# Kernel tuning notes

Hardware: AMD Instinct MI355X
Metric: run time of the kernel (lower is better)

## Reference

```python
import jax, jax.numpy as jnp
import numpy as np

D_MODEL = 1024
NUM_HEADS = 16
D_K = D_MODEL // NUM_HEADS
SCALE = float(np.sqrt(D_K))


def setup_inputs() -> dict:
    key = jax.random.key(0)
    ks = jax.random.split(key, 6)
    x = jax.random.normal(ks[0], (2, 2048, D_MODEL), dtype=jnp.float32)
    s = 1.0 / np.sqrt(D_MODEL)
    w_q = jax.random.uniform(ks[1], (D_MODEL, D_MODEL), jnp.float32, -s, s)
    w_k = jax.random.uniform(ks[2], (D_MODEL, D_MODEL), jnp.float32, -s, s)
    w_v = jax.random.uniform(ks[3], (D_MODEL, D_MODEL), jnp.float32, -s, s)
    w_o = jax.random.uniform(ks[4], (D_MODEL, D_MODEL), jnp.float32, -s, s)
    b_o = jax.random.uniform(ks[5], (D_MODEL,), jnp.float32, -s, s)
    return {"x": x, "w_q": w_q, "w_k": w_k, "w_v": w_v, "w_o": w_o, "b_o": b_o}


def reference(x, w_q, w_k, w_v, w_o, b_o):
    B, S, _ = x.shape
    # project and split heads: [B, H, S, d_k]
    def heads(w):
        return (x @ w.T).reshape(B, S, NUM_HEADS, D_K).transpose(0, 2, 1, 3)
    Q, K, V = heads(w_q), heads(w_k), heads(w_v)
    scores = jnp.einsum("bhqd,bhkd->bhqk", Q, K) / SCALE  # [B,H,S,S]
    attn = jax.nn.softmax(scores, axis=-1)
    context = jnp.einsum("bhqk,bhkd->bhqd", attn, V)
    context = context.transpose(0, 2, 1, 3).reshape(B, S, D_MODEL)
    return context @ w_o.T + b_o
```

## Files before the change

kernel.cpp:

```cpp
#include <hip/hip_runtime.h>

typedef unsigned short u16t;
typedef short bf16x8 __attribute__((ext_vector_type(8)));
typedef short bf16x4 __attribute__((ext_vector_type(4)));
typedef float f32x4 __attribute__((ext_vector_type(4)));

#define NHEADS 16
#define SEQ 2048
#define DMODEL 1024
#define HEAD_ELEMS (SEQ * 64)
#define LSTR 72
#define QSTR 40
#define MATE ((size_t)2 * SEQ * DMODEL)
#define CSC 0.1803368801f
#define MB 4.0f

__device__ __forceinline__ u16t f2bf(float f) {
  union { float f; unsigned u; } v; v.f = f;
  unsigned r = v.u + 0x7FFFu + ((v.u >> 16) & 1u);
  return (u16t)(r >> 16);
}
__device__ __forceinline__ float bf2f(u16t b) {
  union { unsigned u; float f; } v; v.u = ((unsigned)b) << 16;
  return v.f;
}
__device__ __forceinline__ float sanef(float x) {
  return fminf(fmaxf(x, -16384.f), 16384.f);
}
__device__ __forceinline__ unsigned pk2(float a, float b) {
  union { float f; unsigned u; } x, y; x.f = a; y.f = b;
  return __builtin_amdgcn_perm(y.u + 0x8000u, x.u + 0x8000u, 0x07060302u);
}
__device__ __forceinline__ bf16x8 cvt8(const float* p) {
  const f32x4* q4 = (const f32x4*)p;
  f32x4 a = q4[0], b = q4[1];
  bf16x8 o;
  o[0] = (short)f2bf(a[0]); o[1] = (short)f2bf(a[1]);
  o[2] = (short)f2bf(a[2]); o[3] = (short)f2bf(a[3]);
  o[4] = (short)f2bf(b[0]); o[5] = (short)f2bf(b[1]);
  o[6] = (short)f2bf(b[2]); o[7] = (short)f2bf(b[3]);
  return o;
}

struct ushort4a { u16t x, y, z, w; } __attribute__((aligned(8)));

__device__ __forceinline__ int detect_bf16_wave(const u16t* p) {
  int lane = threadIdx.x & 63;
  int cnt = 0;
#pragma unroll
  for (int i = 0; i < 8; ++i) {
    int ex = (p[2 * (lane * 8 + i)] >> 7) & 0xFF;
    cnt += (ex >= 100 && ex <= 140) ? 1 : 0;
  }
  cnt += __shfl_xor(cnt, 1);
  cnt += __shfl_xor(cnt, 2);
  cnt += __shfl_xor(cnt, 4);
  cnt += __shfl_xor(cnt, 8);
  cnt += __shfl_xor(cnt, 16);
  cnt += __shfl_xor(cnt, 32);
  return cnt >= 300;
}

__global__ __launch_bounds__(256, 3) void qkv_kernel(
    const void* __restrict__ xv,
    const void* __restrict__ wqv, const void* __restrict__ wkv,
    const void* __restrict__ wvv,
    u16t* __restrict__ q_ws, u16t* __restrict__ k_ws, u16t* __restrict__ vt_ws) {
  __shared__ u16t As[2][128 * QSTR];
  __shared__ u16t Bs[2][128 * QSTR];
  const int bfm = detect_bf16_wave((const u16t*)xv);
  const int tid = threadIdx.x;
  const int bm0 = blockIdx.x * 128;
  const int bn0 = blockIdx.y * 128;
  const int z = blockIdx.z;
  const void* Wv = (z == 0) ? wqv : ((z == 1) ? wkv : wvv);
  const float scale = (z == 0) ? CSC : 1.0f;
  const int lane = tid & 63;
  const int w = tid >> 6;
  const int ln = lane & 15;
  const int quad = lane >> 4;
  const int wm = (w & 1) * 64;
  const int wn = (w >> 1) * 64;

  f32x4 acc[4][4] = {};

  auto do_mfma = [&](int cur) {
    bf16x8 a[4], b[4];
#pragma unroll
    for (int t = 0; t < 4; ++t)
      a[t] = *(const bf16x8*)&As[cur][(wm + t * 16 + ln) * QSTR + quad * 8];
#pragma unroll
    for (int t = 0; t < 4; ++t)
      b[t] = *(const bf16x8*)&Bs[cur][(wn + t * 16 + ln) * QSTR + quad * 8];
    if (z < 2) {
#pragma unroll
      for (int p = 0; p < 4; ++p)
#pragma unroll
        for (int q = 0; q < 4; ++q)
          acc[p][q] = __builtin_amdgcn_mfma_f32_16x16x32_bf16(b[p], a[q], acc[p][q], 0, 0, 0);
    } else {
#pragma unroll
      for (int p = 0; p < 4; ++p)
#pragma unroll
        for (int q = 0; q < 4; ++q)
          acc[p][q] = __builtin_amdgcn_mfma_f32_16x16x32_bf16(a[p], b[q], acc[p][q], 0, 0, 0);
    }
  };

  if (bfm) {
    const u16t* x = (const u16t*)xv;
    const u16t* W = (const u16t*)Wv;
    const int c0 = tid, c1 = tid + 256;
    const int r0 = c0 >> 2, o0 = (c0 & 3) * 8;
    const int r1 = c1 >> 2, o1 = (c1 & 3) * 8;
    const u16t* xa0 = x + (size_t)(bm0 + r0) * DMODEL + o0;
    const u16t* xa1 = x + (size_t)(bm0 + r1) * DMODEL + o1;
    const u16t* wb0 = W + (size_t)(bn0 + r0) * DMODEL + o0;
    const u16t* wb1 = W + (size_t)(bn0 + r1) * DMODEL + o1;
    const int d0 = r0 * QSTR + o0, d1 = r1 * QSTR + o1;

    bf16x8 ra0 = *(const bf16x8*)xa0, ra1 = *(const bf16x8*)xa1;
    bf16x8 rb0 = *(const bf16x8*)wb0, rb1 = *(const bf16x8*)wb1;
    *(bf16x8*)&As[0][d0] = ra0; *(bf16x8*)&As[0][d1] = ra1;
    *(bf16x8*)&Bs[0][d0] = rb0; *(bf16x8*)&Bs[0][d1] = rb1;
    __syncthreads();
    for (int kt = 0; kt < 32; ++kt) {
      int cur = kt & 1;
      if (kt < 31) {
        xa0 += 32; xa1 += 32; wb0 += 32; wb1 += 32;
        ra0 = *(const bf16x8*)xa0; ra1 = *(const bf16x8*)xa1;
        rb0 = *(const bf16x8*)wb0; rb1 = *(const bf16x8*)wb1;
      }
      do_mfma(cur);
      if (kt < 31) {
        int nxt = cur ^ 1;
        *(bf16x8*)&As[nxt][d0] = ra0; *(bf16x8*)&As[nxt][d1] = ra1;
        *(bf16x8*)&Bs[nxt][d0] = rb0; *(bf16x8*)&Bs[nxt][d1] = rb1;
        __syncthreads();
      }
    }
  } else {
    const float* x = (const float*)xv;
    const float* W = (const float*)Wv;
    for (int kt = 0; kt < 32; ++kt) {
      __syncthreads();
#pragma unroll
      for (int j = 0; j < 2; ++j) {
        int c = j * 256 + tid;
        int row = c >> 2, col = (c & 3) * 8;
        *(bf16x8*)&As[0][row * QSTR + col] = cvt8(x + (size_t)(bm0 + row) * DMODEL + kt * 32 + col);
        *(bf16x8*)&Bs[0][row * QSTR + col] = cvt8(W + (size_t)(bn0 + row) * DMODEL + kt * 32 + col);
      }
      __syncthreads();
      do_mfma(0);
    }
  }

  if (z < 2) {
    u16t* dst = (z == 0) ? q_ws : k_ws;
#pragma unroll
    for (int p = 0; p < 4; ++p) {
      int n_base = bn0 + wn + p * 16 + quad * 4;
      int h = n_base >> 6, dkb = n_base & 63;
#pragma unroll
      for (int q = 0; q < 4; ++q) {
        int m = bm0 + wm + q * 16 + ln;
        int bb = m >> 11, sq = m & 2047;
        ushort4a pk;
        pk.x = f2bf(sanef(acc[p][q][0]) * scale);
        pk.y = f2bf(sanef(acc[p][q][1]) * scale);
        pk.z = f2bf(sanef(acc[p][q][2]) * scale);
        pk.w = f2bf(sanef(acc[p][q][3]) * scale);
        *(ushort4a*)&dst[(size_t)(bb * NHEADS + h) * HEAD_ELEMS + sq * 64 + dkb] = pk;
      }
    }
  } else {
#pragma unroll
    for (int p = 0; p < 4; ++p) {
      int m_base = bm0 + wm + p * 16 + quad * 4;
      int bb = m_base >> 11, sq = m_base & 2047;
#pragma unroll
      for (int q = 0; q < 4; ++q) {
        int n = bn0 + wn + q * 16 + ln;
        int h = n >> 6, dk = n & 63;
        ushort4a pk;
        pk.x = f2bf(sanef(acc[p][q][0]));
        pk.y = f2bf(sanef(acc[p][q][1]));
        pk.z = f2bf(sanef(acc[p][q][2]));
        pk.w = f2bf(sanef(acc[p][q][3]));
        *(ushort4a*)&vt_ws[(size_t)(bb * NHEADS + h) * HEAD_ELEMS + (size_t)dk * SEQ + sq] = pk;
      }
    }
  }
}

__global__ __launch_bounds__(512, 4) void attn_kernel(
    const u16t* __restrict__ q_ws, const u16t* __restrict__ k_ws,
    const u16t* __restrict__ vt_ws, u16t* __restrict__ ctx_ws) {
  __shared__ u16t Ks[2][64 * LSTR];
  __shared__ u16t Vt[2][64 * LSTR];
  const int tid = threadIdx.x;
  const int w = tid >> 6;
  const int lane = tid & 63;
  const int ln = lane & 15;
  const int quad = lane >> 4;
  const int bh = blockIdx.y;
  const size_t base = (size_t)bh * HEAD_ELEMS;
  const int q0w = blockIdx.x * 128 + w * 16;

  bf16x8 aq[2];
#pragma unroll
  for (int ks = 0; ks < 2; ++ks)
    aq[ks] = *(const bf16x8*)(q_ws + base + (size_t)(q0w + ln) * 64 + ks * 32 + quad * 8);

  const int r = tid >> 3;
  const int cc = (tid & 7) * 8;
  const int d = r * LSTR + cc;
  const u16t* kp = k_ws + base + (size_t)tid * 8;
  const u16t* vp = vt_ws + base + (size_t)r * SEQ + cc;

  f32x4 accO[4] = {};
  float psum = 0.f;

  bf16x8 rk = *(const bf16x8*)kp;
  bf16x8 rv = *(const bf16x8*)vp;
  *(bf16x8*)&Ks[0][d] = rk;
  *(bf16x8*)&Vt[0][d] = rv;
  __syncthreads();

  for (int kt = 0; kt < 32; ++kt) {
    const int cur = kt & 1;
    if (kt < 31) {
      kp += 4096; vp += 64;
      rk = *(const bf16x8*)kp;
      rv = *(const bf16x8*)vp;
    }

    f32x4 st[4];
#pragma unroll
    for (int nt = 0; nt < 4; ++nt) {
      st[nt][0] = -MB; st[nt][1] = -MB; st[nt][2] = -MB; st[nt][3] = -MB;
    }
#pragma unroll
    for (int nt = 0; nt < 4; ++nt)
#pragma unroll
      for (int ks = 0; ks < 2; ++ks) {
        bf16x8 bk = *(const bf16x8*)&Ks[cur][(nt * 16 + ln) * LSTR + ks * 32 + quad * 8];
        st[nt] = __builtin_amdgcn_mfma_f32_16x16x32_bf16(bk, aq[ks], st[nt], 0, 0, 0);
      }

#pragma unroll
    for (int pp = 0; pp < 2; ++pp) {
      float pv[8];
#pragma unroll
      for (int j = 0; j < 4; ++j) {
        pv[j]     = exp2f(st[2 * pp][j]);
        pv[4 + j] = exp2f(st[2 * pp + 1][j]);
      }
      psum += ((pv[0] + pv[1]) + (pv[2] + pv[3])) + ((pv[4] + pv[5]) + (pv[6] + pv[7]));
      union { unsigned u[4]; bf16x8 v; } ap;
      ap.u[0] = pk2(pv[0], pv[1]);
      ap.u[1] = pk2(pv[2], pv[3]);
      ap.u[2] = pk2(pv[4], pv[5]);
      ap.u[3] = pk2(pv[6], pv[7]);
#pragma unroll
      for (int dt = 0; dt < 4; ++dt) {
        const u16t* vrow = &Vt[cur][(dt * 16 + ln) * LSTR + quad * 4];
        bf16x4 lo = *(const bf16x4*)(vrow + (2 * pp) * 16);
        bf16x4 hi = *(const bf16x4*)(vrow + (2 * pp + 1) * 16);
        bf16x8 bb = __builtin_shufflevector(lo, hi, 0, 1, 2, 3, 4, 5, 6, 7);
        accO[dt] = __builtin_amdgcn_mfma_f32_16x16x32_bf16(ap.v, bb, accO[dt], 0, 0, 0);
      }
    }

    if (kt < 31) {
      const int nxt = cur ^ 1;
      *(bf16x8*)&Ks[nxt][d] = rk;
      *(bf16x8*)&Vt[nxt][d] = rv;
      __syncthreads();
    }
  }

  psum += __shfl_xor(psum, 16);
  psum += __shfl_xor(psum, 32);
  float inv[4];
#pragma unroll
  for (int rr = 0; rr < 4; ++rr) {
    float lq = __shfl(psum, quad * 4 + rr);
    inv[rr] = 1.0f / fmaxf(lq, 1e-20f);
  }
#pragma unroll
  for (int dt = 0; dt < 4; ++dt)
#pragma unroll
    for (int rr = 0; rr < 4; ++rr)
      ctx_ws[base + (size_t)(q0w + quad * 4 + rr) * 64 + dt * 16 + ln] =
          f2bf(accO[dt][rr] * inv[rr]);
}

__global__ __launch_bounds__(256, 4) void outproj_kernel(
    const u16t* __restrict__ ctx, const void* __restrict__ wov,
    const void* __restrict__ bov_, void* __restrict__ outv) {
  __shared__ u16t As[2][64 * LSTR];
  __shared__ u16t Bs[2][64 * LSTR];
  const int bfm = detect_bf16_wave((const u16t*)wov);
  const int tid = threadIdx.x;
  const int bm0 = blockIdx.x * 64;
  const int bn0 = blockIdx.y * 64;
  const int lane = tid & 63;
  const int w = tid >> 6;
  const int ln = lane & 15;
  const int quad = lane >> 4;
  const int wm = (w & 1) * 32;
  const int wn = (w >> 1) * 32;

  f32x4 acc[2][2] = {};

  auto do_mfma = [&](int cur) {
    bf16x8 a[2][2], b[2][2];
#pragma unroll
    for (int t = 0; t < 2; ++t)
#pragma unroll
      for (int ks = 0; ks < 2; ++ks) {
        a[t][ks] = *(const bf16x8*)&As[cur][(wm + t * 16 + ln) * LSTR + ks * 32 + quad * 8];
        b[t][ks] = *(const bf16x8*)&Bs[cur][(wn + t * 16 + ln) * LSTR + ks * 32 + quad * 8];
      }
#pragma unroll
    for (int p = 0; p < 2; ++p)
#pragma unroll
      for (int q = 0; q < 2; ++q)
#pragma unroll
        for (int ks = 0; ks < 2; ++ks)
          acc[p][q] = __builtin_amdgcn_mfma_f32_16x16x32_bf16(b[p][ks], a[q][ks], acc[p][q], 0, 0, 0);
  };

  const int c0 = tid, c1 = tid + 256;
  const int r0 = c0 >> 3, o0 = (c0 & 7) * 8;
  const int r1 = c1 >> 3, o1 = (c1 & 7) * 8;
  const int d0 = r0 * LSTR + o0, d1 = r1 * LSTR + o1;
  const int m0 = bm0 + r0, m1 = bm0 + r1;
  const u16t* ap0 = ctx + (size_t)((m0 >> 11) * NHEADS) * HEAD_ELEMS + (m0 & 2047) * 64 + o0;
  const u16t* ap1 = ctx + (size_t)((m1 >> 11) * NHEADS) * HEAD_ELEMS + (m1 & 2047) * 64 + o1;

  if (bfm) {
    const u16t* wo = (const u16t*)wov;
    const u16t* bp0 = wo + (size_t)(bn0 + r0) * DMODEL + o0;
    const u16t* bp1 = wo + (size_t)(bn0 + r1) * DMODEL + o1;
    bf16x8 ra0 = *(const bf16x8*)ap0, ra1 = *(const bf16x8*)ap1;
    bf16x8 rb0 = *(const bf16x8*)bp0, rb1 = *(const bf16x8*)bp1;
    *(bf16x8*)&As[0][d0] = ra0; *(bf16x8*)&As[0][d1] = ra1;
    *(bf16x8*)&Bs[0][d0] = rb0; *(bf16x8*)&Bs[0][d1] = rb1;
    __syncthreads();
    for (int kt = 0; kt < 16; ++kt) {
      int cur = kt & 1;
      if (kt < 15) {
        ap0 += HEAD_ELEMS; ap1 += HEAD_ELEMS;
        bp0 += 64; bp1 += 64;
        ra0 = *(const bf16x8*)ap0; ra1 = *(const bf16x8*)ap1;
        rb0 = *(const bf16x8*)bp0; rb1 = *(const bf16x8*)bp1;
      }
      do_mfma(cur);
      if (kt < 15) {
        int nxt = cur ^ 1;
        *(bf16x8*)&As[nxt][d0] = ra0; *(bf16x8*)&As[nxt][d1] = ra1;
        *(bf16x8*)&Bs[nxt][d0] = rb0; *(bf16x8*)&Bs[nxt][d1] = rb1;
        __syncthreads();
      }
    }
  } else {
    const float* wo = (const float*)wov;
    for (int kt = 0; kt < 16; ++kt) {
      __syncthreads();
      *(bf16x8*)&As[0][d0] = *(const bf16x8*)(ap0 + (size_t)kt * HEAD_ELEMS);
      *(bf16x8*)&As[0][d1] = *(const bf16x8*)(ap1 + (size_t)kt * HEAD_ELEMS);
      *(bf16x8*)&Bs[0][d0] = cvt8(wo + (size_t)(bn0 + r0) * DMODEL + kt * 64 + o0);
      *(bf16x8*)&Bs[0][d1] = cvt8(wo + (size_t)(bn0 + r1) * DMODEL + kt * 64 + o1);
      __syncthreads();
      do_mfma(0);
    }
  }

#pragma unroll
  for (int p = 0; p < 2; ++p) {
    int n_base = bn0 + wn + p * 16 + quad * 4;
    float bv0, bv1, bv2, bv3;
    if (bfm) {
      ushort4a bb = *(const ushort4a*)&((const u16t*)bov_)[n_base];
      bv0 = bf2f(bb.x); bv1 = bf2f(bb.y); bv2 = bf2f(bb.z); bv3 = bf2f(bb.w);
    } else {
      const float* bf = (const float*)bov_;
      bv0 = bf[n_base]; bv1 = bf[n_base + 1]; bv2 = bf[n_base + 2]; bv3 = bf[n_base + 3];
    }
#pragma unroll
    for (int q = 0; q < 2; ++q) {
      int m = bm0 + wm + q * 16 + ln;
      float v0 = sanef(acc[p][q][0]) + bv0;
      float v1 = sanef(acc[p][q][1]) + bv1;
      float v2 = sanef(acc[p][q][2]) + bv2;
      float v3 = sanef(acc[p][q][3]) + bv3;
      if (bfm) {
        ushort4a pk; pk.x = f2bf(v0); pk.y = f2bf(v1); pk.z = f2bf(v2); pk.w = f2bf(v3);
        *(ushort4a*)&((u16t*)outv)[(size_t)m * DMODEL + n_base] = pk;
      } else {
        f32x4 pk; pk[0] = v0; pk[1] = v1; pk[2] = v2; pk[3] = v3;
        *(f32x4*)&((float*)outv)[(size_t)m * DMODEL + n_base] = pk;
      }
    }
  }
}

extern "C" void kernel_launch(void* const* d_in, const int* in_sizes, int n_in,
                              void* d_out, int out_size, void* d_ws, size_t ws_size,
                              hipStream_t stream) {
  (void)in_sizes; (void)n_in; (void)out_size; (void)ws_size;
  const void* x  = d_in[0];
  const void* wq = d_in[1];
  const void* wk = d_in[2];
  const void* wv = d_in[3];
  const void* wo = d_in[4];
  const void* bo = d_in[5];

  u16t* q_ws  = (u16t*)d_ws;
  u16t* k_ws  = q_ws + MATE;
  u16t* vt_ws = k_ws + MATE;
  u16t* ctx_ws = q_ws;

  dim3 gA(32, 8, 3);
  qkv_kernel<<<gA, 256, 0, stream>>>(x, wq, wk, wv, q_ws, k_ws, vt_ws);

  dim3 gB(16, 32);
  attn_kernel<<<gB, 512, 0, stream>>>(q_ws, k_ws, vt_ws, ctx_ws);

  dim3 gC(64, 16);
  outproj_kernel<<<gC, 256, 0, stream>>>(ctx_ws, wo, bo, d_out);
}
```

Before: 234.7 us.

## Retile out-projection to 128x128 with direct global-to-LDS loads, single-buffer attention

The output projection moves from 64x64 to 128x128 tiles with K-step 32. It loads A and B straight into LDS through global_load_lds, raising data reuse per block and removing register staging. The attention kernel drops its LDS double buffering in favour of a single buffer with two barriers per tile, which cuts shared memory use but exposes global load latency. The qkv launch bounds rise to 4 waves per SIMD for occupancy. These changes trade fewer blocks and less pipelining for larger tiles and lower LDS pressure.

Result: slower. 550.6 us (+134.6%).

```diff
diff --git a/kernel.cpp b/kernel.cpp
--- a/kernel.cpp
+++ b/kernel.cpp
@@ -42,6 +42,12 @@
   return o;
 }
 
+__device__ __forceinline__ void stage16(const u16t* g, u16t* l) {
+  __builtin_amdgcn_global_load_lds(
+      (const __attribute__((address_space(1))) unsigned int*)g,
+      (__attribute__((address_space(3))) unsigned int*)l, 16, 0, 0);
+}
+
 struct ushort4a { u16t x, y, z, w; } __attribute__((aligned(8)));
 
 __device__ __forceinline__ int detect_bf16_wave(const u16t* p) {
@@ -61,7 +67,7 @@
   return cnt >= 300;
 }
 
-__global__ __launch_bounds__(256, 3) void qkv_kernel(
+__global__ __launch_bounds__(256, 4) void qkv_kernel(
     const void* __restrict__ xv,
     const void* __restrict__ wqv, const void* __restrict__ wkv,
     const void* __restrict__ wvv,
@@ -197,8 +203,8 @@
 __global__ __launch_bounds__(512, 4) void attn_kernel(
     const u16t* __restrict__ q_ws, const u16t* __restrict__ k_ws,
     const u16t* __restrict__ vt_ws, u16t* __restrict__ ctx_ws) {
-  __shared__ u16t Ks[2][64 * LSTR];
-  __shared__ u16t Vt[2][64 * LSTR];
+  __shared__ u16t Ks[64 * LSTR];
+  __shared__ u16t Vt[64 * LSTR];
   const int tid = threadIdx.x;
   const int w = tid >> 6;
   const int lane = tid & 63;
@@ -215,26 +221,21 @@
 
   const int r = tid >> 3;
   const int cc = (tid & 7) * 8;
-  const int d = r * LSTR + cc;
   const u16t* kp = k_ws + base + (size_t)tid * 8;
   const u16t* vp = vt_ws + base + (size_t)r * SEQ + cc;
+  u16t* kl = &Ks[r * LSTR + cc];
+  u16t* vl = &Vt[r * LSTR + cc];
 
   f32x4 accO[4] = {};
   float psum = 0.f;
 
-  bf16x8 rk = *(const bf16x8*)kp;
-  bf16x8 rv = *(const bf16x8*)vp;
-  *(bf16x8*)&Ks[0][d] = rk;
-  *(bf16x8*)&Vt[0][d] = rv;
-  __syncthreads();
-
   for (int kt = 0; kt < 32; ++kt) {
-    const int cur = kt & 1;
-    if (kt < 31) {
-      kp += 4096; vp += 64;
-      rk = *(const bf16x8*)kp;
-      rv = *(const bf16x8*)vp;
-    }
+    bf16x8 rk = *(const bf16x8*)kp; kp += 4096;
+    bf16x8 rv = *(const bf16x8*)vp; vp += 64;
+    __syncthreads();
+    *(bf16x8*)kl = rk;
+    *(bf16x8*)vl = rv;
+    __syncthreads();
 
     f32x4 st[4];
 #pragma unroll
@@ -245,7 +246,7 @@
     for (int nt = 0; nt < 4; ++nt)
 #pragma unroll
       for (int ks = 0; ks < 2; ++ks) {
-        bf16x8 bk = *(const bf16x8*)&Ks[cur][(nt * 16 + ln) * LSTR + ks * 32 + quad * 8];
+        bf16x8 bk = *(const bf16x8*)&Ks[(nt * 16 + ln) * LSTR + ks * 32 + quad * 8];
         st[nt] = __builtin_amdgcn_mfma_f32_16x16x32_bf16(bk, aq[ks], st[nt], 0, 0, 0);
       }
 
@@ -265,20 +266,13 @@
       ap.u[3] = pk2(pv[6], pv[7]);
 #pragma unroll
       for (int dt = 0; dt < 4; ++dt) {
-        const u16t* vrow = &Vt[cur][(dt * 16 + ln) * LSTR + quad * 4];
+        const u16t* vrow = &Vt[(dt * 16 + ln) * LSTR + quad * 4];
         bf16x4 lo = *(const bf16x4*)(vrow + (2 * pp) * 16);
         bf16x4 hi = *(const bf16x4*)(vrow + (2 * pp + 1) * 16);
         bf16x8 bb = __builtin_shufflevector(lo, hi, 0, 1, 2, 3, 4, 5, 6, 7);
         accO[dt] = __builtin_amdgcn_mfma_f32_16x16x32_bf16(ap.v, bb, accO[dt], 0, 0, 0);
       }
     }
-
-    if (kt < 31) {
-      const int nxt = cur ^ 1;
-      *(bf16x8*)&Ks[nxt][d] = rk;
-      *(bf16x8*)&Vt[nxt][d] = rv;
-      __syncthreads();
-    }
   }
 
   psum += __shfl_xor(psum, 16);
@@ -297,90 +291,59 @@
           f2bf(accO[dt][rr] * inv[rr]);
 }
 
-__global__ __launch_bounds__(256, 4) void outproj_kernel(
+__global__ __launch_bounds__(256) void outproj_kernel(
     const u16t* __restrict__ ctx, const void* __restrict__ wov,
     const void* __restrict__ bov_, void* __restrict__ outv) {
-  __shared__ u16t As[2][64 * LSTR];
-  __shared__ u16t Bs[2][64 * LSTR];
+  __shared__ u16t As[128 * 32];
+  __shared__ u16t Bs[128 * 32];
   const int bfm = detect_bf16_wave((const u16t*)wov);
   const int tid = threadIdx.x;
-  const int bm0 = blockIdx.x * 64;
-  const int bn0 = blockIdx.y * 64;
+  const int bm0 = blockIdx.x * 128;
+  const int bn0 = blockIdx.y * 128;
   const int lane = tid & 63;
   const int w = tid >> 6;
   const int ln = lane & 15;
   const int quad = lane >> 4;
-  const int wm = (w & 1) * 32;
-  const int wn = (w >> 1) * 32;
-
-  f32x4 acc[2][2] = {};
-
-  auto do_mfma = [&](int cur) {
-    bf16x8 a[2][2], b[2][2];
-#pragma unroll
-    for (int t = 0; t < 2; ++t)
-#pragma unroll
-      for (int ks = 0; ks < 2; ++ks) {
-        a[t][ks] = *(const bf16x8*)&As[cur][(wm + t * 16 + ln) * LSTR + ks * 32 + quad * 8];
-        b[t][ks] = *(const bf16x8*)&Bs[cur][(wn + t * 16 + ln) * LSTR + ks * 32 + quad * 8];
-      }
-#pragma unroll
-    for (int p = 0; p < 2; ++p)
-#pragma unroll
-      for (int q = 0; q < 2; ++q)
-#pragma unroll
-        for (int ks = 0; ks < 2; ++ks)
-          acc[p][q] = __builtin_amdgcn_mfma_f32_16x16x32_bf16(b[p][ks], a[q][ks], acc[p][q], 0, 0, 0);
-  };
-
-  const int c0 = tid, c1 = tid + 256;
-  const int r0 = c0 >> 3, o0 = (c0 & 7) * 8;
-  const int r1 = c1 >> 3, o1 = (c1 & 7) * 8;
-  const int d0 = r0 * LSTR + o0, d1 = r1 * LSTR + o1;
-  const int m0 = bm0 + r0, m1 = bm0 + r1;
-  const u16t* ap0 = ctx + (size_t)((m0 >> 11) * NHEADS) * HEAD_ELEMS + (m0 & 2047) * 64 + o0;
-  const u16t* ap1 = ctx + (size_t)((m1 >> 11) * NHEADS) * HEAD_ELEMS + (m1 & 2047) * 64 + o1;
-
-  if (bfm) {
-    const u16t* wo = (const u16t*)wov;
-    const u16t* bp0 = wo + (size_t)(bn0 + r0) * DMODEL + o0;
-    const u16t* bp1 = wo + (size_t)(bn0 + r1) * DMODEL + o1;
-    bf16x8 ra0 = *(const bf16x8*)ap0, ra1 = *(const bf16x8*)ap1;
-    bf16x8 rb0 = *(const bf16x8*)bp0, rb1 = *(const bf16x8*)bp1;
-    *(bf16x8*)&As[0][d0] = ra0; *(bf16x8*)&As[0][d1] = ra1;
-    *(bf16x8*)&Bs[0][d0] = rb0; *(bf16x8*)&Bs[0][d1] = rb1;
-    __syncthreads();
-    for (int kt = 0; kt < 16; ++kt) {
-      int cur = kt & 1;
-      if (kt < 15) {
-        ap0 += HEAD_ELEMS; ap1 += HEAD_ELEMS;
-        bp0 += 64; bp1 += 64;
-        ra0 = *(const bf16x8*)ap0; ra1 = *(const bf16x8*)ap1;
-        rb0 = *(const bf16x8*)bp0; rb1 = *(const bf16x8*)bp1;
-      }
-      do_mfma(cur);
-      if (kt < 15) {
-        int nxt = cur ^ 1;
-        *(bf16x8*)&As[nxt][d0] = ra0; *(bf16x8*)&As[nxt][d1] = ra1;
-        *(bf16x8*)&Bs[nxt][d0] = rb0; *(bf16x8*)&Bs[nxt][d1] = rb1;
-        __syncthreads();
-      }
-    }
-  } else {
-    const float* wo = (const float*)wov;
-    for (int kt = 0; kt < 16; ++kt) {
-      __syncthreads();
-      *(bf16x8*)&As[0][d0] = *(const bf16x8*)(ap0 + (size_t)kt * HEAD_ELEMS);
-      *(bf16x8*)&As[0][d1] = *(const bf16x8*)(ap1 + (size_t)kt * HEAD_ELEMS);
-      *(bf16x8*)&Bs[0][d0] = cvt8(wo + (size_t)(bn0 + r0) * DMODEL + kt * 64 + o0);
-      *(bf16x8*)&Bs[0][d1] = cvt8(wo + (size_t)(bn0 + r1) * DMODEL + kt * 64 + o1);
-      __syncthreads();
-      do_mfma(0);
-    }
-  }
-
-#pragma unroll
-  for (int p = 0; p < 2; ++p) {
+  const int wm = (w & 1) * 64;
+  const int wn = (w >> 1) * 64;
+
+  f32x4 acc[4][4] = {};
+
+  for (int kt = 0; kt < 32; ++kt) {
+    __syncthreads();
+#pragma unroll
+    for (int j = 0; j < 2; ++j) {
+      int f = j * 256 + tid;
+      int row = f >> 2;
+      int col = (f & 3) * 8;
+      int m = bm0 + row;
+      int bb = m >> 11, s = m & 2047;
+      int k = kt * 32 + col;
+      int h = k >> 6, dk = k & 63;
+      stage16(ctx + (size_t)(bb * NHEADS + h) * HEAD_ELEMS + s * 64 + dk, &As[f * 8]);
+      if (bfm) {
+        stage16((const u16t*)wov + (size_t)(bn0 + row) * DMODEL + kt * 32 + col, &Bs[f * 8]);
+      } else {
+        *(bf16x8*)&Bs[f * 8] = cvt8((const float*)wov + (size_t)(bn0 + row) * DMODEL + kt * 32 + col);
+      }
+    }
+    __syncthreads();
+    bf16x8 a[4], b[4];
+#pragma unroll
+    for (int t = 0; t < 4; ++t)
+      a[t] = *(const bf16x8*)&As[(wm + t * 16 + ln) * 32 + quad * 8];
+#pragma unroll
+    for (int t = 0; t < 4; ++t)
+      b[t] = *(const bf16x8*)&Bs[(wn + t * 16 + ln) * 32 + quad * 8];
+#pragma unroll
+    for (int p = 0; p < 4; ++p)
+#pragma unroll
+      for (int q = 0; q < 4; ++q)
+        acc[p][q] = __builtin_amdgcn_mfma_f32_16x16x32_bf16(b[p], a[q], acc[p][q], 0, 0, 0);
+  }
+
+#pragma unroll
+  for (int p = 0; p < 4; ++p) {
     int n_base = bn0 + wn + p * 16 + quad * 4;
     float bv0, bv1, bv2, bv3;
     if (bfm) {
@@ -391,7 +354,7 @@
       bv0 = bf[n_base]; bv1 = bf[n_base + 1]; bv2 = bf[n_base + 2]; bv3 = bf[n_base + 3];
     }
 #pragma unroll
-    for (int q = 0; q < 2; ++q) {
+    for (int q = 0; q < 4; ++q) {
       int m = bm0 + wm + q * 16 + ln;
       float v0 = sanef(acc[p][q][0]) + bv0;
       float v1 = sanef(acc[p][q][1]) + bv1;
@@ -430,6 +393,6 @@
   dim3 gB(16, 32);
   attn_kernel<<<gB, 512, 0, stream>>>(q_ws, k_ws, vt_ws, ctx_ws);
 
-  dim3 gC(64, 16);
+  dim3 gC(32, 8);
   outproj_kernel<<<gC, 256, 0, stream>>>(ctx_ws, wo, bo, d_out);
 }
```
